# Optimization experiments

Hardware: AMD Instinct MI355X
Metric: run time of the kernel (lower is better)

## Reference

```python
import jax, jax.numpy as jnp
import numpy as np

EPS = 1e-5

def conv1x1(x, w, b):
    # x: [B,Cin,H,W], w: [Cout,Cin], b: [Cout]
    return jnp.einsum('oi,bihw->bohw', w, x) + b[None, :, None, None]

def self_attention(x, qw, qb, kw, kb, vw, vb, fw, fb):
    B, C, H, W = x.shape
    hid = qw.shape[0]
    q = conv1x1(x, qw, qb).reshape(B, hid, H * W).transpose(0, 2, 1)   # [B,HW,hid]
    k = conv1x1(x, kw, kb).reshape(B, hid, H * W)                      # [B,hid,HW]
    v = conv1x1(x, vw, vb).reshape(B, C, H * W)                        # [B,C,HW]
    attn = jax.nn.softmax(jnp.einsum('bnh,bhm->bnm', q, k), axis=-1)   # [B,HW,HW]
    z = jnp.einsum('bnm,bcm->bnc', attn, v)                            # [B,HW,C]
    # faithful to torch .view(B,C,H,W) on contiguous [B,HW,C]: raw reshape, no transpose
    z = z.reshape(B, C, H, W)
    return conv1x1(z * x, fw, fb) + x

def group_norm_per_channel(y, gw, gb):
    # GroupNorm(num_groups == num_channels): per-channel instance norm, biased var
    mean = y.mean(axis=(2, 3), keepdims=True)
    var = ((y - mean) ** 2).mean(axis=(2, 3), keepdims=True)
    yn = (y - mean) * jax.lax.rsqrt(var + EPS)
    return yn * gw[None, :, None, None] + gb[None, :, None, None]

def setup_inputs() -> dict:
    key = jax.random.key(0)
    ks = jax.random.split(key, 32)
    B, C, H, W = 4, 64, 64, 64
    hid, att = 64, 64
    d = {}
    d['x'] = jax.random.normal(ks[0], (B, C, H, W), jnp.float32)
    d['h'] = jax.random.normal(ks[1], (B, hid, H, W), jnp.float32)
    d['c'] = jax.random.normal(ks[2], (B, hid, H, W), jnp.float32)
    i = 3
    for pre, cin in (('ax', C), ('ah', hid)):
        for nm, cout in (('q', att), ('k', att), ('v', cin), ('f', cin)):
            d[f'{pre}_{nm}w'] = jax.random.normal(ks[i], (cout, cin), jnp.float32) * 0.05; i += 1
            d[f'{pre}_{nm}b'] = jax.random.normal(ks[i], (cout,), jnp.float32) * 0.05; i += 1
    d['conv_w'] = jax.random.normal(ks[i], (4 * hid, C + hid, 3, 3), jnp.float32) * 0.05; i += 1
    d['conv_b'] = jax.random.normal(ks[i], (4 * hid,), jnp.float32) * 0.05; i += 1
    d['gn_w'] = jnp.ones((4 * hid,), jnp.float32)
    d['gn_b'] = jnp.zeros((4 * hid,), jnp.float32)
    return d

def reference(x, h, c,
              ax_qw, ax_qb, ax_kw, ax_kb, ax_vw, ax_vb, ax_fw, ax_fb,
              ah_qw, ah_qb, ah_kw, ah_kb, ah_vw, ah_vb, ah_fw, ah_fb,
              conv_w, conv_b, gn_w, gn_b):
    hid = h.shape[1]
    xa = self_attention(x, ax_qw, ax_qb, ax_kw, ax_kb, ax_vw, ax_vb, ax_fw, ax_fb)
    ha = self_attention(h, ah_qw, ah_qb, ah_kw, ah_kb, ah_vw, ah_vb, ah_fw, ah_fb)
    combined = jnp.concatenate([xa, ha], axis=1)
    y = jax.lax.conv_general_dilated(
        combined, conv_w, window_strides=(1, 1), padding=[(1, 1), (1, 1)],
        dimension_numbers=('NCHW', 'OIHW', 'NCHW')) + conv_b[None, :, None, None]
    y = group_norm_per_channel(y, gn_w, gn_b)
    i, f, o, g = jnp.split(y, 4, axis=1)
    i = jax.nn.sigmoid(i); f = jax.nn.sigmoid(f); o = jax.nn.sigmoid(o); g = jnp.tanh(g)
    c_next = f * c + i * g
    h_next = o * jnp.tanh(c_next)
    return jnp.stack([h_next, c_next])  # [2,B,hid,H,W]
```

## Files before the change

kernel.cpp:

```cpp
#include <hip/hip_runtime.h>
#include <hip/hip_bf16.h>


typedef __hip_bfloat16 bf16;
typedef const __hip_bfloat16* bfp;
typedef short bf16x8 __attribute__((ext_vector_type(8)));
typedef short short4v __attribute__((ext_vector_type(4)));
typedef float f32x4 __attribute__((ext_vector_type(4)));

#define SM_SHIFT 12.0f

__device__ __forceinline__ float ldf(const void* p, long i, int f32) {
    return f32 ? ((const float*)p)[i]
               : __bfloat162float(((const bf16*)p)[i]);
}
__device__ __forceinline__ short f2bf(float f) {
    bf16 h = __float2bfloat16(f);
    return *reinterpret_cast<short*>(&h);
}

__global__ void sniff_kernel(const void* __restrict__ x, int* __restrict__ flag)
{
    const unsigned short* u = (const unsigned short*)x;
    int lane = threadIdx.x;
    int ok = 0;
    for (int i = 0; i < 4; ++i) {
        int e = (u[lane * 4 + i] >> 7) & 0xFF;
        ok += (e >= 100 && e <= 141);
    }
    ok += __shfl_xor(ok, 1, 64);
    ok += __shfl_xor(ok, 2, 64);
    ok += __shfl_xor(ok, 4, 64);
    ok += __shfl_xor(ok, 8, 64);
    ok += __shfl_xor(ok, 16, 64);
    ok += __shfl_xor(ok, 32, 64);
    if (lane == 0) *flag = (ok < 200) ? 1 : 0;
}

__global__ __launch_bounds__(256) void wt_kernel(
    const void* __restrict__ cw, bf16* __restrict__ Wt,
    float* __restrict__ gacc, const int* __restrict__ flag)
{
    if (blockIdx.x == 0) {
        for (int j = 0; j < 8; ++j)
            gacc[threadIdx.x * 8 + j] = 0.f;
    }
    int f32 = *flag;
    int idx = blockIdx.x * 256 + threadIdx.x;
    int tap = idx >> 15;
    int rem = idx & 32767;
    int oc = rem >> 7, ic = rem & 127;
    Wt[idx] = __float2bfloat16(ldf(cw, ((long)oc * 128 + ic) * 9 + tap, f32));
}

__global__ __launch_bounds__(256) void qkv_kernel(
    const void* __restrict__ Xx, const void* __restrict__ Xh,
    const void* __restrict__ qwx, const void* __restrict__ qbx,
    const void* __restrict__ kwx, const void* __restrict__ kbx,
    const void* __restrict__ vwx, const void* __restrict__ vbx,
    const void* __restrict__ qwh, const void* __restrict__ qbh,
    const void* __restrict__ kwh, const void* __restrict__ kbh,
    const void* __restrict__ vwh, const void* __restrict__ vbh,
    bf16* __restrict__ Qx, bf16* __restrict__ Kx, bf16* __restrict__ Vtx,
    bf16* __restrict__ Qh, bf16* __restrict__ Kh, bf16* __restrict__ Vth,
    const int* __restrict__ flag)
{
    __shared__ __align__(16) short xt[64][72];
    __shared__ __align__(16) short wq[64][72];
    __shared__ __align__(16) short wk[64][72];
    __shared__ __align__(16) short wv[64][72];
    int ab  = blockIdx.x >> 8;
    int idx = blockIdx.x & 255;
    int b = idx >> 6;
    int n0 = (idx & 63) * 64;
    int tid = threadIdx.x;
    int wave = tid >> 6, lane = tid & 63;
    int q = lane >> 4, l15 = lane & 15;
    int f32 = *flag;

    const void* X = ab ? Xh : Xx;
    const void* qw = ab ? qwh : qwx; const void* qb = ab ? qbh : qbx;
    const void* kw = ab ? kwh : kwx; const void* kb = ab ? kbh : kbx;
    const void* vw = ab ? vwh : vwx; const void* vb = ab ? vbh : vbx;
    short* Qg  = (short*)(ab ? Qh  : Qx)  + (long)b * 262144;
    short* Kg  = (short*)(ab ? Kh  : Kx)  + (long)b * 262144;
    short* Vtg = (short*)(ab ? Vth : Vtx) + (long)b * 262144;

    if (!f32) {
        const short* q16 = (const short*)qw;
        const short* k16 = (const short*)kw;
        const short* v16 = (const short*)vw;
        for (int rep = 0; rep < 2; ++rep) {
            int j8 = (rep * 256 + tid) * 8;
            *(bf16x8*)&wq[j8 >> 6][j8 & 63] = *(const bf16x8*)(q16 + j8);
            *(bf16x8*)&wk[j8 >> 6][j8 & 63] = *(const bf16x8*)(k16 + j8);
            *(bf16x8*)&wv[j8 >> 6][j8 & 63] = *(const bf16x8*)(v16 + j8);
        }
    } else {
        for (int rep = 0; rep < 16; ++rep) {
            int j = rep * 256 + tid;
            int i = j >> 6, cc = j & 63;
            wq[i][cc] = f2bf(((const float*)qw)[j]);
            wk[i][cc] = f2bf(((const float*)kw)[j]);
            wv[i][cc] = f2bf(((const float*)vw)[j]);
        }
    }
    long xbase = (long)b * 262144;
    for (int rep = 0; rep < 16; ++rep) {
        int c = rep * 4 + (tid >> 6);
        int p = tid & 63;
        xt[p][c] = f2bf(ldf(X, xbase + (long)c * 4096 + n0 + p, f32));
    }
    __syncthreads();

    bf16x8 a0 = *(const bf16x8*)&xt[wave * 16 + l15][q * 8];
    bf16x8 a1 = *(const bf16x8*)&xt[wave * 16 + l15][32 + q * 8];

    for (int ct = 0; ct < 4; ++ct) {
        bf16x8 bq0 = *(const bf16x8*)&wq[ct * 16 + l15][q * 8];
        bf16x8 bq1 = *(const bf16x8*)&wq[ct * 16 + l15][32 + q * 8];
        f32x4 z = (f32x4){0.f, 0.f, 0.f, 0.f};
        z = __builtin_amdgcn_mfma_f32_16x16x32_bf16(a0, bq0, z, 0, 0, 0);
        z = __builtin_amdgcn_mfma_f32_16x16x32_bf16(a1, bq1, z, 0, 0, 0);
        float bias = ldf(qb, ct * 16 + l15, f32);
        for (int reg = 0; reg < 4; ++reg)
            Qg[(long)(n0 + wave * 16 + q * 4 + reg) * 64 + ct * 16 + l15] =
                f2bf(z[reg] + bias);
    }
    for (int ct = 0; ct < 4; ++ct) {
        bf16x8 bk0 = *(const bf16x8*)&wk[ct * 16 + l15][q * 8];
        bf16x8 bk1 = *(const bf16x8*)&wk[ct * 16 + l15][32 + q * 8];
        f32x4 z = (f32x4){0.f, 0.f, 0.f, 0.f};
        z = __builtin_amdgcn_mfma_f32_16x16x32_bf16(a0, bk0, z, 0, 0, 0);
        z = __builtin_amdgcn_mfma_f32_16x16x32_bf16(a1, bk1, z, 0, 0, 0);
        float bias = ldf(kb, ct * 16 + l15, f32);
        for (int reg = 0; reg < 4; ++reg)
            Kg[(long)(n0 + wave * 16 + q * 4 + reg) * 64 + ct * 16 + l15] =
                f2bf(z[reg] + bias);
    }
    bf16x8 av0 = *(const bf16x8*)&wv[wave * 16 + l15][q * 8];
    bf16x8 av1 = *(const bf16x8*)&wv[wave * 16 + l15][32 + q * 8];
    for (int ct = 0; ct < 4; ++ct) {
        bf16x8 bx0 = *(const bf16x8*)&xt[ct * 16 + l15][q * 8];
        bf16x8 bx1 = *(const bf16x8*)&xt[ct * 16 + l15][32 + q * 8];
        f32x4 z = (f32x4){0.f, 0.f, 0.f, 0.f};
        z = __builtin_amdgcn_mfma_f32_16x16x32_bf16(av0, bx0, z, 0, 0, 0);
        z = __builtin_amdgcn_mfma_f32_16x16x32_bf16(av1, bx1, z, 0, 0, 0);
        for (int reg = 0; reg < 4; ++reg) {
            int c_out = wave * 16 + q * 4 + reg;
            float bias = ldf(vb, c_out, f32);
            Vtg[(long)c_out * 4096 + n0 + ct * 16 + l15] = f2bf(z[reg] + bias);
        }
    }
}

__global__ __launch_bounds__(256, 2) void attn_kernel(
    bfp Qx, bfp Kx, bfp Vtx, bf16* Ox,
    bfp Qh, bfp Kh, bfp Vth, bf16* Oh,
    float* __restrict__ lw, int split)
{
    __shared__ __align__(16) short ks [2][64][64];
    __shared__ __align__(16) short vts[2][64][64];
    __shared__ __align__(16) short ps[4][16][64];
    int tid = threadIdx.x;
    int wave = tid >> 6, lane = tid & 63;
    int q = lane >> 4, l15 = lane & 15;
    int idx = blockIdx.x & 255;
    int ab, half, mstart, ntile;
    if (split) {
        ab = blockIdx.x >> 9; half = (blockIdx.x >> 8) & 1;
        mstart = half * 2048; ntile = 32;
    } else {
        ab = blockIdx.x >> 8; half = 0; mstart = 0; ntile = 64;
    }
    int b = idx >> 6;
    int rt = idx & 63;
    int n0 = rt * 64 + wave * 16;
    const short* Qb  = (const short*)(ab ? Qh  : Qx)  + (long)b * 262144;
    const short* Kb  = (const short*)(ab ? Kh  : Kx)  + (long)b * 262144;
    const short* Vtb = (const short*)(ab ? Vth : Vtx) + (long)b * 262144;
    short* Ob = (short*)(ab ? Oh : Ox) + (long)half * (1l << 20) + (long)b * 262144;

    bf16x8 aq0 = *(const bf16x8*)(Qb + (long)(n0 + l15) * 64 + q * 8);
    bf16x8 aq1 = *(const bf16x8*)(Qb + (long)(n0 + l15) * 64 + 32 + q * 8);

    f32x4 acc_o[4];
    for (int ct = 0; ct < 4; ++ct) acc_o[ct] = (f32x4){0.f, 0.f, 0.f, 0.f};
    float l_part[4] = {0.f, 0.f, 0.f, 0.f};

    int swp = (l15 >> 1) & 7;
    int c0 = (q ^ swp) << 3;
    int c1 = ((q + 4) ^ swp) << 3;
    int sw_s = (tid >> 4) & 7;
    int cs = (((tid & 7) ^ sw_s)) << 3;

    int r0 = tid >> 3, r1 = r0 + 32;
    bf16x8 pk0 = *(const bf16x8*)(Kb + (long)(mstart + r0) * 64 + (tid & 7) * 8);
    bf16x8 pk1 = *(const bf16x8*)(Kb + (long)(mstart + r1) * 64 + (tid & 7) * 8);
    bf16x8 pv0 = *(const bf16x8*)(Vtb + (long)r0 * 4096 + mstart + (tid & 7) * 8);
    bf16x8 pv1 = *(const bf16x8*)(Vtb + (long)r1 * 4096 + mstart + (tid & 7) * 8);

    for (int it = 0; it < ntile; ++it) {
        int buf = it & 1;
        *(bf16x8*)&ks[buf][r0][cs]  = pk0;
        *(bf16x8*)&ks[buf][r1][cs]  = pk1;
        *(bf16x8*)&vts[buf][r0][cs] = pv0;
        *(bf16x8*)&vts[buf][r1][cs] = pv1;
        __syncthreads();
        if (it + 1 < ntile) {
            long m = (long)mstart + (long)(it + 1) * 64;
            pk0 = *(const bf16x8*)(Kb + (m + r0) * 64 + (tid & 7) * 8);
            pk1 = *(const bf16x8*)(Kb + (m + r1) * 64 + (tid & 7) * 8);
            pv0 = *(const bf16x8*)(Vtb + (long)r0 * 4096 + m + (tid & 7) * 8);
            pv1 = *(const bf16x8*)(Vtb + (long)r1 * 4096 + m + (tid & 7) * 8);
        }

        f32x4 s[4];
        for (int t = 0; t < 4; ++t) {
            const short* krow = &ks[buf][t * 16 + l15][0];
            bf16x8 bk0 = *(const bf16x8*)(krow + c0);
            bf16x8 bk1 = *(const bf16x8*)(krow + c1);
            f32x4 z = (f32x4){0.f, 0.f, 0.f, 0.f};
            z    = __builtin_amdgcn_mfma_f32_16x16x32_bf16(aq0, bk0, z, 0, 0, 0);
            s[t] = __builtin_amdgcn_mfma_f32_16x16x32_bf16(aq1, bk1, z, 0, 0, 0);
        }

        for (int t = 0; t < 4; ++t) {
            int chunkbase = t << 1 | (l15 >> 3);
            for (int reg = 0; reg < 4; ++reg) {
                float p = __expf(fminf(s[t][reg] - SM_SHIFT, 60.f));
                l_part[reg] += p;
                int n = q * 4 + reg;
                int swn = (n >> 1) & 7;
                ps[wave][n][((chunkbase ^ swn) << 3) | (l15 & 7)] = f2bf(p);
            }
        }

        const short* prow = &ps[wave][l15][0];
        bf16x8 bp0 = *(const bf16x8*)(prow + c0);
        bf16x8 bp1 = *(const bf16x8*)(prow + c1);
        for (int ct = 0; ct < 4; ++ct) {
            const short* vrow = &vts[buf][ct * 16 + l15][0];
            bf16x8 av0 = *(const bf16x8*)(vrow + c0);
            bf16x8 av1 = *(const bf16x8*)(vrow + c1);
            acc_o[ct] = __builtin_amdgcn_mfma_f32_16x16x32_bf16(av0, bp0, acc_o[ct], 0, 0, 0);
            acc_o[ct] = __builtin_amdgcn_mfma_f32_16x16x32_bf16(av1, bp1, acc_o[ct], 0, 0, 0);
        }
    }

    for (int reg = 0; reg < 4; ++reg) {
        l_part[reg] += __shfl_xor(l_part[reg], 1, 64);
        l_part[reg] += __shfl_xor(l_part[reg], 2, 64);
        l_part[reg] += __shfl_xor(l_part[reg], 4, 64);
        l_part[reg] += __shfl_xor(l_part[reg], 8, 64);
    }
    if (split) {
        if (l15 == 0) {
            float* lp = lw + (long)ab * 32768 + (long)half * 16384
                           + (long)b * 4096 + n0 + q * 4;
            lp[0] = l_part[0]; lp[1] = l_part[1];
            lp[2] = l_part[2]; lp[3] = l_part[3];
        }
        for (int ct = 0; ct < 4; ++ct) {
            short* dst = Ob + (long)(n0 + l15) * 64 + ct * 16 + q * 4;
            dst[0] = f2bf(acc_o[ct][0]);
            dst[1] = f2bf(acc_o[ct][1]);
            dst[2] = f2bf(acc_o[ct][2]);
            dst[3] = f2bf(acc_o[ct][3]);
        }
    } else {
        int src = (l15 >> 2) << 4;
        float L0 = __shfl(l_part[0], src, 64);
        float L1 = __shfl(l_part[1], src, 64);
        float L2 = __shfl(l_part[2], src, 64);
        float L3 = __shfl(l_part[3], src, 64);
        int r3 = l15 & 3;
        float ln = (r3 == 0) ? L0 : (r3 == 1) ? L1 : (r3 == 2) ? L2 : L3;
        float iln = 1.f / ln;
        for (int ct = 0; ct < 4; ++ct) {
            short* dst = Ob + (long)(n0 + l15) * 64 + ct * 16 + q * 4;
            dst[0] = f2bf(acc_o[ct][0] * iln);
            dst[1] = f2bf(acc_o[ct][1] * iln);
            dst[2] = f2bf(acc_o[ct][2] * iln);
            dst[3] = f2bf(acc_o[ct][3] * iln);
        }
    }
}

__global__ __launch_bounds__(256) void attnout_kernel(
    bfp Ox, const void* __restrict__ Xx,
    const void* __restrict__ fwx, const void* __restrict__ fbx,
    bf16* __restrict__ outx,
    bfp Oh, const void* __restrict__ Xh,
    const void* __restrict__ fwh, const void* __restrict__ fbh,
    bf16* __restrict__ outh,
    const float* __restrict__ lw, int split,
    const int* __restrict__ flag)
{
    __shared__ __align__(16) short fwt[64][72];
    __shared__ __align__(16) short at [64][72];
    int f32 = *flag;
    int ab  = blockIdx.x >> 8;
    int idx = blockIdx.x & 255;
    int b = idx >> 6;
    int h = idx & 63;
    int tid = threadIdx.x;
    int wave = tid >> 6, lane = tid & 63;
    int q = lane >> 4, l15 = lane & 15;
    bfp O = ab ? Oh : Ox;
    const void* X = ab ? Xh : Xx;
    const void* fw = ab ? fwh : fwx;
    const void* fb = ab ? fbh : fbx;
    bf16* out = ab ? outh : outx;

    if (!f32) {
        const short* f16p = (const short*)fw;
        for (int rep = 0; rep < 2; ++rep) {
            int j8 = (rep * 256 + tid) * 8;
            *(bf16x8*)&fwt[j8 >> 6][j8 & 63] = *(const bf16x8*)(f16p + j8);
        }
    } else {
        for (int rep = 0; rep < 16; ++rep) {
            int j = rep * 256 + tid;
            fwt[j >> 6][j & 63] = f2bf(((const float*)fw)[j]);
        }
    }
    const bf16* Ob0 = O + (long)b * 262144;
    const bf16* Ob1 = Ob0 + (1l << 20);
    const float* lp0 = lw + (long)ab * 32768 + (long)b * 4096;
    const float* lp1 = lp0 + 16384;
    long xbase = (long)b * 262144;
    {
        int w = tid & 63;
        for (int rep = 0; rep < 16; ++rep) {
            int cn = rep * 4 + (tid >> 6);
            int n = cn * 64 + h;
            float o;
            if (split) {
                float iln = 1.f / (lp0[n] + lp1[n]);
                o = (__bfloat162float(Ob0[(long)n * 64 + w]) +
                     __bfloat162float(Ob1[(long)n * 64 + w])) * iln;
            } else {
                o = __bfloat162float(Ob0[(long)n * 64 + w]);
            }
            float prod = o * ldf(X, xbase + (long)cn * 4096 + h * 64 + w, f32);
            at[w][cn] = f2bf(prod);
        }
    }
    __syncthreads();
    bf16x8 a0 = *(const bf16x8*)&fwt[wave * 16 + l15][q * 8];
    bf16x8 a1 = *(const bf16x8*)&fwt[wave * 16 + l15][32 + q * 8];
    short* outp = (short*)out;
    for (int nt = 0; nt < 4; ++nt) {
        bf16x8 b0 = *(const bf16x8*)&at[nt * 16 + l15][q * 8];
        bf16x8 b1 = *(const bf16x8*)&at[nt * 16 + l15][32 + q * 8];
        f32x4 z = (f32x4){0.f, 0.f, 0.f, 0.f};
        z = __builtin_amdgcn_mfma_f32_16x16x32_bf16(a0, b0, z, 0, 0, 0);
        z = __builtin_amdgcn_mfma_f32_16x16x32_bf16(a1, b1, z, 0, 0, 0);
        int w = nt * 16 + l15;
        short4v o4;
        for (int reg = 0; reg < 4; ++reg) {
            int o = wave * 16 + q * 4 + reg;
            float v = z[reg] + ldf(fb, o, f32) +
                      ldf(X, xbase + (long)o * 4096 + h * 64 + w, f32);
            o4[reg] = f2bf(v);
        }
        *(short4v*)(outp + (((long)(b * 64 + h) * 64 + w) * 64 + wave * 16 + q * 4)) = o4;
    }
}

__global__ __launch_bounds__(256) void conv3x3_kernel(
    bfp xa, bfp ha, bfp Wt, const void* __restrict__ cb,
    bf16* __restrict__ y, float* __restrict__ gacc,
    const int* __restrict__ flag)
{
    __shared__ __align__(16) short in_s[3][66][136];
    int f32 = *flag;
    int b = blockIdx.x >> 6;
    int h = blockIdx.x & 63;
    int tid = threadIdx.x;
    int wave = tid >> 6, lane = tid & 63;
    int q = lane >> 4, l15 = lane & 15;

    const short* xab = (const short*)xa + (long)b * 262144;
    const short* hab = (const short*)ha + (long)b * 262144;
    const bf16x8 zv = {0, 0, 0, 0, 0, 0, 0, 0};
    for (int r = 0; r < 3; ++r) {
        int gy = h + r - 1;
        bool valid = (gy >= 0) && (gy < 64);
        for (int s = 0; s < 2; ++s) {
            int strip = s * 256 + tid;
            int w = strip >> 3;
            int c8 = (strip & 7) * 8;
            bf16x8 vx = zv, vh = zv;
            if (valid) {
                vx = *(const bf16x8*)(xab + ((long)gy * 64 + w) * 64 + c8);
                vh = *(const bf16x8*)(hab + ((long)gy * 64 + w) * 64 + c8);
            }
            *(bf16x8*)&in_s[r][w + 1][c8]      = vx;
            *(bf16x8*)&in_s[r][w + 1][64 + c8] = vh;
        }
    }
    if (tid < 96) {
        int r = tid / 32;
        int rest = tid % 32;
        int col = (rest & 1) ? 65 : 0;
        int c8 = (rest >> 1) * 8;
        *(bf16x8*)&in_s[r][col][c8] = zv;
    }
    __syncthreads();

    int oc0 = wave * 64;
    f32x4 acc[4][4];
    for (int mt = 0; mt < 4; ++mt)
        for (int nt = 0; nt < 4; ++nt)
            acc[mt][nt] = (f32x4){0.f, 0.f, 0.f, 0.f};

    const short* Wb = (const short*)Wt;
    for (int tap = 0; tap < 9; ++tap) {
        int dy = tap / 3, dx = tap - dy * 3;
        for (int kc = 0; kc < 4; ++kc) {
            bf16x8 afrag[4];
            for (int mt = 0; mt < 4; ++mt)
                afrag[mt] = *(const bf16x8*)(
                    Wb + ((long)tap * 256 + oc0 + mt * 16 + l15) * 128 + kc * 32 + q * 8);
            for (int nt = 0; nt < 4; ++nt) {
                bf16x8 bfrag = *(const bf16x8*)&in_s[dy][nt * 16 + l15 + dx][kc * 32 + q * 8];
                for (int mt = 0; mt < 4; ++mt)
                    acc[mt][nt] = __builtin_amdgcn_mfma_f32_16x16x32_bf16(
                        afrag[mt], bfrag, acc[mt][nt], 0, 0, 0);
            }
        }
    }

    long ybase = (long)b * 1048576 + (long)h * 64;
    for (int mt = 0; mt < 4; ++mt) {
        for (int reg = 0; reg < 4; ++reg) {
            int oc = oc0 + mt * 16 + q * 4 + reg;
            float bias = ldf(cb, oc, f32);
            float s = 0.f, s2 = 0.f;
            for (int nt = 0; nt < 4; ++nt) {
                float v = acc[mt][nt][reg] + bias;
                ((short*)y)[ybase + (long)oc * 4096 + nt * 16 + l15] = f2bf(v);
                s += v; s2 = fmaf(v, v, s2);
            }
            s  += __shfl_xor(s,  1, 64);  s2 += __shfl_xor(s2, 1, 64);
            s  += __shfl_xor(s,  2, 64);  s2 += __shfl_xor(s2, 2, 64);
            s  += __shfl_xor(s,  4, 64);  s2 += __shfl_xor(s2, 4, 64);
            s  += __shfl_xor(s,  8, 64);  s2 += __shfl_xor(s2, 8, 64);
            if (l15 == 0) {
                atomicAdd(&gacc[b * 256 + oc], s);
                atomicAdd(&gacc[1024 + b * 256 + oc], s2);
            }
        }
    }
}

__global__ __launch_bounds__(256) void gates_kernel(
    bfp y, const float* __restrict__ gacc,
    const void* __restrict__ gw, const void* __restrict__ gb,
    const void* __restrict__ c_in, void* __restrict__ out,
    const int* __restrict__ flag)
{
    int f32 = *flag;
    int idx = blockIdx.x * 256 + threadIdx.x;
    int b = idx >> 18;
    int r = idx & 262143;
    int ch = r >> 12;
    int pix = r & 4095;
    long ybase = (long)b * 1048576;
    float vals[4];
    for (int g = 0; g < 4; ++g) {
        int cc = g * 64 + ch;
        float mu  = gacc[b * 256 + cc] * (1.f / 4096.f);
        float var = gacc[1024 + b * 256 + cc] * (1.f / 4096.f) - mu * mu;
        float rstd = rsqrtf(fmaxf(var, 0.f) + 1e-5f);
        float v = __bfloat162float(y[ybase + (long)cc * 4096 + pix]);
        v = (v - mu) * rstd * ldf(gw, cc, f32) + ldf(gb, cc, f32);
        vals[g] = v;
    }
    float ig = 1.f / (1.f + __expf(-vals[0]));
    float fg = 1.f / (1.f + __expf(-vals[1]));
    float og = 1.f / (1.f + __expf(-vals[2]));
    float gg = tanhf(vals[3]);
    float cprev = ldf(c_in, idx, f32);
    float cn = fg * cprev + ig * gg;
    float hn = og * tanhf(cn);
    if (f32) {
        float* o32 = (float*)out;
        o32[idx] = hn;
        o32[1048576 + idx] = cn;
    } else {
        bf16* o16 = (bf16*)out;
        o16[idx] = __float2bfloat16(hn);
        o16[1048576 + idx] = __float2bfloat16(cn);
    }
}

extern "C" void kernel_launch(void* const* d_in, const int* in_sizes, int n_in,
                              void* d_out, int out_size, void* d_ws, size_t ws_size,
                              hipStream_t stream)
{
    const void* x = d_in[0]; const void* h = d_in[1]; const void* c = d_in[2];
    const void* ax_qw = d_in[3],  *ax_qb = d_in[4];
    const void* ax_kw = d_in[5],  *ax_kb = d_in[6];
    const void* ax_vw = d_in[7],  *ax_vb = d_in[8];
    const void* ax_fw = d_in[9],  *ax_fb = d_in[10];
    const void* ah_qw = d_in[11], *ah_qb = d_in[12];
    const void* ah_kw = d_in[13], *ah_kb = d_in[14];
    const void* ah_vw = d_in[15], *ah_vb = d_in[16];
    const void* ah_fw = d_in[17], *ah_fb = d_in[18];
    const void* conv_w = d_in[19], *conv_b = d_in[20];
    const void* gn_w = d_in[21],  *gn_b = d_in[22];

    char* wsb = (char*)d_ws;
    auto S = [&](int i) { return wsb + ((unsigned long)i << 21); };
    bool splitm = ws_size >= (27ul << 20);
    bool fused  = splitm || ws_size >= (18ul << 20) + 16384;

    bf16* ha = (bf16*)S(0);
    bf16* Wt = (bf16*)S(1);
    bf16 *Qx, *Kx, *Vtx, *Qh, *Kh, *Vth, *xa, *y, *Ox, *Oh;
    char* tail;
    if (splitm) {
        Qx = (bf16*)S(2); Kx = (bf16*)S(3); Vtx = (bf16*)S(4);
        Qh = (bf16*)S(5); Kh = (bf16*)S(6); Vth = (bf16*)S(7);
        xa = (bf16*)S(8);
        Ox = (bf16*)S(9);
        Oh = (bf16*)S(11);
        y = Qx;
        tail = S(13);
    } else if (fused) {
        Qx = (bf16*)S(2); Kx = (bf16*)S(3); Vtx = (bf16*)S(4);
        Qh = (bf16*)S(5); Kh = (bf16*)S(6); Vth = (bf16*)S(7);
        xa = (bf16*)S(8); Ox = Qx; Oh = Qh; y = Qx;
        tail = S(9);
    } else {
        Qx = (bf16*)S(2); Kx = (bf16*)S(3); Vtx = (bf16*)S(4);
        Qh = Qx; Kh = Kx; Vth = Vtx;
        xa = (bf16*)S(6); Ox = Qx; Oh = Qh; y = Qx;
        tail = S(7);
    }
    int*  flag = (int*)tail;
    float* gacc = (float*)(tail + 256);
    float* lw   = (float*)(tail + 256 + 8192);

    sniff_kernel<<<1, 64, 0, stream>>>(x, flag);

    if (fused) {
        qkv_kernel<<<512, 256, 0, stream>>>(
            x, h,
            ax_qw, ax_qb, ax_kw, ax_kb, ax_vw, ax_vb,
            ah_qw, ah_qb, ah_kw, ah_kb, ah_vw, ah_vb,
            Qx, Kx, Vtx, Qh, Kh, Vth, flag);
        if (splitm) {
            attn_kernel<<<1024, 256, 0, stream>>>(
                Qx, Kx, Vtx, Ox, Qh, Kh, Vth, Oh, lw, 1);
            attnout_kernel<<<512, 256, 0, stream>>>(
                Ox, x, ax_fw, ax_fb, xa, Oh, h, ah_fw, ah_fb, ha, lw, 1, flag);
        } else {
            attn_kernel<<<512, 256, 0, stream>>>(
                Qx, Kx, Vtx, Ox, Qh, Kh, Vth, Oh, lw, 0);
            attnout_kernel<<<512, 256, 0, stream>>>(
                Ox, x, ax_fw, ax_fb, xa, Oh, h, ah_fw, ah_fb, ha, lw, 0, flag);
        }
    } else {
        qkv_kernel<<<256, 256, 0, stream>>>(
            x, x,
            ax_qw, ax_qb, ax_kw, ax_kb, ax_vw, ax_vb,
            ax_qw, ax_qb, ax_kw, ax_kb, ax_vw, ax_vb,
            Qx, Kx, Vtx, Qx, Kx, Vtx, flag);
        attn_kernel<<<256, 256, 0, stream>>>(
            Qx, Kx, Vtx, Ox, Qx, Kx, Vtx, Ox, lw, 0);
        attnout_kernel<<<256, 256, 0, stream>>>(
            Ox, x, ax_fw, ax_fb, xa, Ox, x, ax_fw, ax_fb, xa, lw, 0, flag);
        qkv_kernel<<<256, 256, 0, stream>>>(
            h, h,
            ah_qw, ah_qb, ah_kw, ah_kb, ah_vw, ah_vb,
            ah_qw, ah_qb, ah_kw, ah_kb, ah_vw, ah_vb,
            Qh, Kh, Vth, Qh, Kh, Vth, flag);
        attn_kernel<<<256, 256, 0, stream>>>(
            Qh, Kh, Vth, Oh, Qh, Kh, Vth, Oh, lw, 0);
        attnout_kernel<<<256, 256, 0, stream>>>(
            Oh, h, ah_fw, ah_fb, ha, Oh, h, ah_fw, ah_fb, ha, lw, 0, flag);
    }
    wt_kernel<<<1152, 256, 0, stream>>>(conv_w, Wt, gacc, flag);
    conv3x3_kernel<<<256, 256, 0, stream>>>(xa, ha, Wt, conv_b, y, gacc, flag);
    gates_kernel<<<4096, 256, 0, stream>>>(y, gacc, gn_w, gn_b, c, d_out, flag);
}
```

Measured before the change: 239.4 us.

## Inline dtype sniff, fold weight transpose into qkv launch, split conv3x3 output channels

Drops the separate sniff kernel and weight-transpose kernel. Each kernel now detects the input dtype itself, and the conv weight reorder and gacc zeroing run as extra blocks of the qkv launch. The conv3x3 grid doubles, with each block computing half the output channels, to improve occupancy. This removes two launches and gives conv more parallelism, at the cost of the halo load being repeated per half and the sniff being recomputed in every block.

```diff
diff --git a/kernel.cpp b/kernel.cpp
--- a/kernel.cpp
+++ b/kernel.cpp
@@ -19,13 +19,14 @@
     return *reinterpret_cast<short*>(&h);
 }
 
-__global__ void sniff_kernel(const void* __restrict__ x, int* __restrict__ flag)
-{
-    const unsigned short* u = (const unsigned short*)x;
-    int lane = threadIdx.x;
+__device__ __forceinline__ int sniff_f32(const void* xr)
+{
+    int lane = threadIdx.x & 63;
+    unsigned long long v = ((const unsigned long long*)xr)[lane];
     int ok = 0;
+#pragma unroll
     for (int i = 0; i < 4; ++i) {
-        int e = (u[lane * 4 + i] >> 7) & 0xFF;
+        int e = (int)((v >> (16 * i + 7)) & 0xFF);
         ok += (e >= 100 && e <= 141);
     }
     ok += __shfl_xor(ok, 1, 64);
@@ -34,23 +35,7 @@
     ok += __shfl_xor(ok, 8, 64);
     ok += __shfl_xor(ok, 16, 64);
     ok += __shfl_xor(ok, 32, 64);
-    if (lane == 0) *flag = (ok < 200) ? 1 : 0;
-}
-
-__global__ __launch_bounds__(256) void wt_kernel(
-    const void* __restrict__ cw, bf16* __restrict__ Wt,
-    float* __restrict__ gacc, const int* __restrict__ flag)
-{
-    if (blockIdx.x == 0) {
-        for (int j = 0; j < 8; ++j)
-            gacc[threadIdx.x * 8 + j] = 0.f;
-    }
-    int f32 = *flag;
-    int idx = blockIdx.x * 256 + threadIdx.x;
-    int tap = idx >> 15;
-    int rem = idx & 32767;
-    int oc = rem >> 7, ic = rem & 127;
-    Wt[idx] = __float2bfloat16(ldf(cw, ((long)oc * 128 + ic) * 9 + tap, f32));
+    return ok < 200;
 }
 
 __global__ __launch_bounds__(256) void qkv_kernel(
@@ -63,20 +48,34 @@
     const void* __restrict__ vwh, const void* __restrict__ vbh,
     bf16* __restrict__ Qx, bf16* __restrict__ Kx, bf16* __restrict__ Vtx,
     bf16* __restrict__ Qh, bf16* __restrict__ Kh, bf16* __restrict__ Vth,
-    const int* __restrict__ flag)
-{
+    const void* __restrict__ cw, bf16* __restrict__ Wt,
+    float* __restrict__ gacc, int qkvN)
+{
+    int bx = blockIdx.x;
+    int tid = threadIdx.x;
+    int f32 = sniff_f32(Xx);
+    if (bx >= qkvN) {
+        if (bx == qkvN) {
+            for (int j = 0; j < 8; ++j)
+                gacc[tid * 8 + j] = 0.f;
+        }
+        int wi = (bx - qkvN) * 256 + tid;
+        int tap = wi >> 15;
+        int rem = wi & 32767;
+        int oc = rem >> 7, ic = rem & 127;
+        Wt[wi] = __float2bfloat16(ldf(cw, ((long)oc * 128 + ic) * 9 + tap, f32));
+        return;
+    }
     __shared__ __align__(16) short xt[64][72];
     __shared__ __align__(16) short wq[64][72];
     __shared__ __align__(16) short wk[64][72];
     __shared__ __align__(16) short wv[64][72];
-    int ab  = blockIdx.x >> 8;
-    int idx = blockIdx.x & 255;
+    int ab  = (bx >> 8) & 1;
+    int idx = bx & 255;
     int b = idx >> 6;
     int n0 = (idx & 63) * 64;
-    int tid = threadIdx.x;
     int wave = tid >> 6, lane = tid & 63;
     int q = lane >> 4, l15 = lane & 15;
-    int f32 = *flag;
 
     const void* X = ab ? Xh : Xx;
     const void* qw = ab ? qwh : qwx; const void* qb = ab ? qbh : qbx;
@@ -294,12 +293,11 @@
     bfp Oh, const void* __restrict__ Xh,
     const void* __restrict__ fwh, const void* __restrict__ fbh,
     bf16* __restrict__ outh,
-    const float* __restrict__ lw, int split,
-    const int* __restrict__ flag)
+    const float* __restrict__ lw, int split)
 {
     __shared__ __align__(16) short fwt[64][72];
     __shared__ __align__(16) short at [64][72];
-    int f32 = *flag;
+    int f32 = sniff_f32(Xx);
     int ab  = blockIdx.x >> 8;
     int idx = blockIdx.x & 255;
     int b = idx >> 6;
@@ -372,12 +370,15 @@
 __global__ __launch_bounds__(256) void conv3x3_kernel(
     bfp xa, bfp ha, bfp Wt, const void* __restrict__ cb,
     bf16* __restrict__ y, float* __restrict__ gacc,
-    const int* __restrict__ flag)
+    const void* __restrict__ xraw)
 {
     __shared__ __align__(16) short in_s[3][66][136];
-    int f32 = *flag;
-    int b = blockIdx.x >> 6;
-    int h = blockIdx.x & 63;
+    int f32 = sniff_f32(xraw);
+    int bx = blockIdx.x;
+    int b = bx >> 7;
+    int rem = bx & 127;
+    int h = rem >> 1;
+    int halfoc = rem & 1;
     int tid = threadIdx.x;
     int wave = tid >> 6, lane = tid & 63;
     int q = lane >> 4, l15 = lane & 15;
@@ -410,9 +411,9 @@
     }
     __syncthreads();
 
-    int oc0 = wave * 64;
-    f32x4 acc[4][4];
-    for (int mt = 0; mt < 4; ++mt)
+    int oc0 = halfoc * 128 + wave * 32;
+    f32x4 acc[2][4];
+    for (int mt = 0; mt < 2; ++mt)
         for (int nt = 0; nt < 4; ++nt)
             acc[mt][nt] = (f32x4){0.f, 0.f, 0.f, 0.f};
 
@@ -420,13 +421,13 @@
     for (int tap = 0; tap < 9; ++tap) {
         int dy = tap / 3, dx = tap - dy * 3;
         for (int kc = 0; kc < 4; ++kc) {
-            bf16x8 afrag[4];
-            for (int mt = 0; mt < 4; ++mt)
+            bf16x8 afrag[2];
+            for (int mt = 0; mt < 2; ++mt)
                 afrag[mt] = *(const bf16x8*)(
                     Wb + ((long)tap * 256 + oc0 + mt * 16 + l15) * 128 + kc * 32 + q * 8);
             for (int nt = 0; nt < 4; ++nt) {
                 bf16x8 bfrag = *(const bf16x8*)&in_s[dy][nt * 16 + l15 + dx][kc * 32 + q * 8];
-                for (int mt = 0; mt < 4; ++mt)
+                for (int mt = 0; mt < 2; ++mt)
                     acc[mt][nt] = __builtin_amdgcn_mfma_f32_16x16x32_bf16(
                         afrag[mt], bfrag, acc[mt][nt], 0, 0, 0);
             }
@@ -434,7 +435,7 @@
     }
 
     long ybase = (long)b * 1048576 + (long)h * 64;
-    for (int mt = 0; mt < 4; ++mt) {
+    for (int mt = 0; mt < 2; ++mt) {
         for (int reg = 0; reg < 4; ++reg) {
             int oc = oc0 + mt * 16 + q * 4 + reg;
             float bias = ldf(cb, oc, f32);
@@ -459,10 +460,9 @@
 __global__ __launch_bounds__(256) void gates_kernel(
     bfp y, const float* __restrict__ gacc,
     const void* __restrict__ gw, const void* __restrict__ gb,
-    const void* __restrict__ c_in, void* __restrict__ out,
-    const int* __restrict__ flag)
-{
-    int f32 = *flag;
+    const void* __restrict__ c_in, void* __restrict__ out)
+{
+    int f32 = sniff_f32(c_in);
     int idx = blockIdx.x * 256 + threadIdx.x;
     int b = idx >> 18;
     int r = idx & 262143;
@@ -541,50 +541,46 @@
         xa = (bf16*)S(6); Ox = Qx; Oh = Qh; y = Qx;
         tail = S(7);
     }
-    int*  flag = (int*)tail;
-    float* gacc = (float*)(tail + 256);
-    float* lw   = (float*)(tail + 256 + 8192);
-
-    sniff_kernel<<<1, 64, 0, stream>>>(x, flag);
+    float* gacc = (float*)tail;
+    float* lw   = (float*)(tail + 8192);
 
     if (fused) {
-        qkv_kernel<<<512, 256, 0, stream>>>(
+        qkv_kernel<<<512 + 1152, 256, 0, stream>>>(
             x, h,
             ax_qw, ax_qb, ax_kw, ax_kb, ax_vw, ax_vb,
             ah_qw, ah_qb, ah_kw, ah_kb, ah_vw, ah_vb,
-            Qx, Kx, Vtx, Qh, Kh, Vth, flag);
+            Qx, Kx, Vtx, Qh, Kh, Vth, conv_w, Wt, gacc, 512);
         if (splitm) {
             attn_kernel<<<1024, 256, 0, stream>>>(
                 Qx, Kx, Vtx, Ox, Qh, Kh, Vth, Oh, lw, 1);
             attnout_kernel<<<512, 256, 0, stream>>>(
-                Ox, x, ax_fw, ax_fb, xa, Oh, h, ah_fw, ah_fb, ha, lw, 1, flag);
+                Ox, x, ax_fw, ax_fb, xa, Oh, h, ah_fw, ah_fb, ha, lw, 1);
         } else {
             attn_kernel<<<512, 256, 0, stream>>>(
                 Qx, Kx, Vtx, Ox, Qh, Kh, Vth, Oh, lw, 0);
             attnout_kernel<<<512, 256, 0, stream>>>(
-                Ox, x, ax_fw, ax_fb, xa, Oh, h, ah_fw, ah_fb, ha, lw, 0, flag);
-        }
-    } else {
-        qkv_kernel<<<256, 256, 0, stream>>>(
+                Ox, x, ax_fw, ax_fb, xa, Oh, h, ah_fw, ah_fb, ha, lw, 0);
+        }
+    } else {
+        qkv_kernel<<<256 + 1152, 256, 0, stream>>>(
             x, x,
             ax_qw, ax_qb, ax_kw, ax_kb, ax_vw, ax_vb,
             ax_qw, ax_qb, ax_kw, ax_kb, ax_vw, ax_vb,
-            Qx, Kx, Vtx, Qx, Kx, Vtx, flag);
+            Qx, Kx, Vtx, Qx, Kx, Vtx, conv_w, Wt, gacc, 256);
         attn_kernel<<<256, 256, 0, stream>>>(
             Qx, Kx, Vtx, Ox, Qx, Kx, Vtx, Ox, lw, 0);
         attnout_kernel<<<256, 256, 0, stream>>>(
-            Ox, x, ax_fw, ax_fb, xa, Ox, x, ax_fw, ax_fb, xa, lw, 0, flag);
+            Ox, x, ax_fw, ax_fb, xa, Ox, x, ax_fw, ax_fb, xa, lw, 0);
         qkv_kernel<<<256, 256, 0, stream>>>(
             h, h,
             ah_qw, ah_qb, ah_kw, ah_kb, ah_vw, ah_vb,
             ah_qw, ah_qb, ah_kw, ah_kb, ah_vw, ah_vb,
-            Qh, Kh, Vth, Qh, Kh, Vth, flag);
+            Qh, Kh, Vth, Qh, Kh, Vth, conv_w, Wt, gacc, 256);
         attn_kernel<<<256, 256, 0, stream>>>(
             Qh, Kh, Vth, Oh, Qh, Kh, Vth, Oh, lw, 0);
         attnout_kernel<<<256, 256, 0, stream>>>(
-            Oh, h, ah_fw, ah_fb, ha, Oh, h, ah_fw, ah_fb, ha, lw, 0, flag);
-    }
-    wt_kernel<<<1152, 256, 0, stream>>>(conv_w, Wt, gacc, flag);
-    conv3x3_kernel<<<256, 256, 0, stream>>>(xa, ha, Wt, conv_b, y, gacc, flag);
-    gates_kernel<<<4096, 256, 0, stream>>>(y, gacc, gn_w, gn_b, c, d_out, flag);
-}
+            Oh, h, ah_fw, ah_fb, ha, Oh, h, ah_fw, ah_fb, ha, lw, 0);
+    }
+    conv3x3_kernel<<<512, 256, 0, stream>>>(xa, ha, Wt, conv_b, y, gacc, x);
+    gates_kernel<<<4096, 256, 0, stream>>>(y, gacc, gn_w, gn_b, c, d_out);
+}
```

Result: no change. 235.5 us (-1.7%).
